# Kernel optimization log

Measured on AMD Instinct MI355X. Metric: run time of the kernel, lower is better.

Reference implementation:

```python
import jax, jax.numpy as jnp
import numpy as np

FDIM = 32
FSIZE = 128          # grid resolution is FSIZE+1 = 129 per axis
N_POINTS = 1048576   # 2**20 query points


def _grid_sample_3d(fm, coords):
    """Trilinear sample of fm [C, D, H, W] at coords [N, 3] in [-1, 1].

    Matches torch F.grid_sample(align_corners=True, padding_mode='border'):
    coords[:, 0] indexes W (x), coords[:, 1] indexes H (y), coords[:, 2] indexes D (z).
    Returns [N, C].
    """
    C, D, H, W = fm.shape

    def prep(c, size):
        # align_corners=True unnormalization, then border clamp
        i = jnp.clip((c + 1.0) * 0.5 * (size - 1), 0.0, size - 1.0)
        i0 = jnp.floor(i)
        idx0 = i0.astype(jnp.int32)
        idx1 = jnp.minimum(idx0 + 1, size - 1)
        return idx0, idx1, i - i0  # frac in [0, 1)

    x0, x1, tx = prep(coords[:, 0], W)
    y0, y1, ty = prep(coords[:, 1], H)
    z0, z1, tz = prep(coords[:, 2], D)

    flat = fm.reshape(C, D * H * W).T  # [D*H*W, C] for point-major gathers

    def gather(zi, yi, xi):
        return jnp.take(flat, (zi * H + yi) * W + xi, axis=0)  # [N, C]

    wx0, wx1 = (1.0 - tx)[:, None], tx[:, None]
    wy0, wy1 = (1.0 - ty)[:, None], ty[:, None]
    wz0, wz1 = (1.0 - tz)[:, None], tz[:, None]

    out = (gather(z0, y0, x0) * (wz0 * wy0 * wx0)
           + gather(z0, y0, x1) * (wz0 * wy0 * wx1)
           + gather(z0, y1, x0) * (wz0 * wy1 * wx0)
           + gather(z0, y1, x1) * (wz0 * wy1 * wx1)
           + gather(z1, y0, x0) * (wz1 * wy0 * wx0)
           + gather(z1, y0, x1) * (wz1 * wy0 * wx1)
           + gather(z1, y1, x0) * (wz1 * wy1 * wx0)
           + gather(z1, y1, x1) * (wz1 * wy1 * wx1))
    return out  # [N, C]


def setup_inputs() -> dict:
    key = jax.random.key(0)
    k1, k2 = jax.random.split(key)
    x = jax.random.uniform(k1, (N_POINTS, 3), jnp.float32, -1.0, 1.0)
    fm = jax.random.normal(k2, (FDIM, FSIZE + 1, FSIZE + 1, FSIZE + 1), jnp.float32) * 0.01
    return {"x": x, "fm": fm}


def reference(x, fm):
    # FeatureVolume.forward with x.shape[1] == 3: returns [N, fdim]
    return _grid_sample_3d(fm, x)
```

## Files before the change

### kernel.cpp

```cpp
#include <hip/hip_runtime.h>
#include <hip/hip_bf16.h>
#include <stdint.h>


#define GRIDW 129
#define S_TOTAL (129 * 129 * 129)
#define NCH 32

typedef float f32x4 __attribute__((ext_vector_type(4)));

static __device__ __forceinline__ ushort f32_to_bf16_rne(float f) {
    uint32_t u = __float_as_uint(f);
    u += 0x7FFFu + ((u >> 16) & 1u);
    return (ushort)(u >> 16);
}

__global__ __launch_bounds__(256) void fv_transpose(const float* __restrict__ fm,
                                                    ushort* __restrict__ vol) {
    __shared__ float tile[256 * 33];
    const int tid = threadIdx.x;
    const int s0 = blockIdx.x * 256;
    const int s = min(s0 + tid, S_TOTAL - 1);
    const float* p = fm + s;
#pragma unroll
    for (int c = 0; c < NCH; ++c) {
        tile[tid * 33 + c] = __builtin_nontemporal_load(p);
        p += S_TOTAL;
    }
    __syncthreads();
    const int sl = tid >> 2;
    const int c0 = (tid & 3) * 8;
#pragma unroll
    for (int k = 0; k < 4; ++k) {
        const int srow = k * 64 + sl;
        const int sg = s0 + srow;
        if (sg < S_TOTAL) {
            uint32_t w[4];
#pragma unroll
            for (int j = 0; j < 4; ++j) {
                const ushort lo = f32_to_bf16_rne(tile[srow * 33 + c0 + 2 * j]);
                const ushort hi = f32_to_bf16_rne(tile[srow * 33 + c0 + 2 * j + 1]);
                w[j] = (uint32_t)lo | ((uint32_t)hi << 16);
            }
            *reinterpret_cast<uint4*>(vol + (size_t)sg * NCH + c0) =
                make_uint4(w[0], w[1], w[2], w[3]);
        }
    }
}

static __device__ __forceinline__ void bf16x4_to_f(uint2 q, float f[4]) {
    f[0] = __uint_as_float(q.x << 16);
    f[1] = __uint_as_float(q.x & 0xFFFF0000u);
    f[2] = __uint_as_float(q.y << 16);
    f[3] = __uint_as_float(q.y & 0xFFFF0000u);
}

__global__ __launch_bounds__(256) void fv_sample(const float* __restrict__ x,
                                                 const ushort* __restrict__ vol,
                                                 float* __restrict__ out,
                                                 int npts) {
    const int gid = blockIdx.x * 256 + threadIdx.x;
    const int p = gid >> 3;
    if (p >= npts) return;
    const int lane8 = gid & 7;

    const float cx = x[3 * p + 0];
    const float cy = x[3 * p + 1];
    const float cz = x[3 * p + 2];

    const float fx = fminf(fmaxf((cx + 1.0f) * 0.5f * 128.0f, 0.0f), 128.0f);
    const float fy = fminf(fmaxf((cy + 1.0f) * 0.5f * 128.0f, 0.0f), 128.0f);
    const float fz = fminf(fmaxf((cz + 1.0f) * 0.5f * 128.0f, 0.0f), 128.0f);

    const float fx0 = floorf(fx), fy0 = floorf(fy), fz0 = floorf(fz);
    const int ix0 = (int)fx0, iy0 = (int)fy0, iz0 = (int)fz0;
    const float tx = fx - fx0, ty = fy - fy0, tz = fz - fz0;
    const uint32_t dX = (ix0 < GRIDW - 1) ? 8u : 0u;
    const uint32_t dY = (iy0 < GRIDW - 1) ? (GRIDW * 8u) : 0u;
    const uint32_t dZ = (iz0 < GRIDW - 1) ? (GRIDW * GRIDW * 8u) : 0u;

    const uint32_t o000 = (uint32_t)((iz0 * GRIDW + iy0) * GRIDW + ix0) * 8u + (uint32_t)lane8;
    const uint32_t o001 = o000 + dX;
    const uint32_t o010 = o000 + dY;
    const uint32_t o011 = o010 + dX;
    const uint32_t o100 = o000 + dZ;
    const uint32_t o101 = o100 + dX;
    const uint32_t o110 = o100 + dY;
    const uint32_t o111 = o110 + dX;

    const uint2* __restrict__ vp = reinterpret_cast<const uint2*>(vol);
    const uint2 q000 = vp[o000];
    const uint2 q001 = vp[o001];
    const uint2 q010 = vp[o010];
    const uint2 q011 = vp[o011];
    const uint2 q100 = vp[o100];
    const uint2 q101 = vp[o101];
    const uint2 q110 = vp[o110];
    const uint2 q111 = vp[o111];

    const float wx1 = tx, wx0 = 1.0f - tx;
    const float wy1 = ty, wy0 = 1.0f - ty;
    const float wz1 = tz, wz0 = 1.0f - tz;
    const float wzy00 = wz0 * wy0, wzy01 = wz0 * wy1;
    const float wzy10 = wz1 * wy0, wzy11 = wz1 * wy1;
    const float w000 = wzy00 * wx0, w001 = wzy00 * wx1;
    const float w010 = wzy01 * wx0, w011 = wzy01 * wx1;
    const float w100 = wzy10 * wx0, w101 = wzy10 * wx1;
    const float w110 = wzy11 * wx0, w111 = wzy11 * wx1;

    float f[4], acc[4];
    bf16x4_to_f(q000, f);
#pragma unroll
    for (int j = 0; j < 4; ++j) acc[j] = w000 * f[j];
    bf16x4_to_f(q001, f);
#pragma unroll
    for (int j = 0; j < 4; ++j) acc[j] += w001 * f[j];
    bf16x4_to_f(q010, f);
#pragma unroll
    for (int j = 0; j < 4; ++j) acc[j] += w010 * f[j];
    bf16x4_to_f(q011, f);
#pragma unroll
    for (int j = 0; j < 4; ++j) acc[j] += w011 * f[j];
    bf16x4_to_f(q100, f);
#pragma unroll
    for (int j = 0; j < 4; ++j) acc[j] += w100 * f[j];
    bf16x4_to_f(q101, f);
#pragma unroll
    for (int j = 0; j < 4; ++j) acc[j] += w101 * f[j];
    bf16x4_to_f(q110, f);
#pragma unroll
    for (int j = 0; j < 4; ++j) acc[j] += w110 * f[j];
    bf16x4_to_f(q111, f);
#pragma unroll
    for (int j = 0; j < 4; ++j) acc[j] += w111 * f[j];

    f32x4 r = {acc[0], acc[1], acc[2], acc[3]};
    f32x4* dst = reinterpret_cast<f32x4*>(out + (size_t)p * NCH) + lane8;
    __builtin_nontemporal_store(r, dst);
}

__global__ __launch_bounds__(256) void fv_sample_direct(const float* __restrict__ x,
                                                        const float* __restrict__ fm,
                                                        float* __restrict__ out,
                                                        int npts) {
    const int gid = blockIdx.x * 256 + threadIdx.x;
    const int p = gid >> 5;
    if (p >= npts) return;
    const int c = gid & 31;

    const float cx = x[3 * p + 0];
    const float cy = x[3 * p + 1];
    const float cz = x[3 * p + 2];

    const float fx = fminf(fmaxf((cx + 1.0f) * 0.5f * 128.0f, 0.0f), 128.0f);
    const float fy = fminf(fmaxf((cy + 1.0f) * 0.5f * 128.0f, 0.0f), 128.0f);
    const float fz = fminf(fmaxf((cz + 1.0f) * 0.5f * 128.0f, 0.0f), 128.0f);

    const float fx0 = floorf(fx), fy0 = floorf(fy), fz0 = floorf(fz);
    const int ix0 = (int)fx0, iy0 = (int)fy0, iz0 = (int)fz0;
    const float tx = fx - fx0, ty = fy - fy0, tz = fz - fz0;
    const int dX = (ix0 < GRIDW - 1) ? 1 : 0;
    const int dY = (iy0 < GRIDW - 1) ? GRIDW : 0;
    const int dZ = (iz0 < GRIDW - 1) ? (GRIDW * GRIDW) : 0;

    const int s000 = (iz0 * GRIDW + iy0) * GRIDW + ix0;
    const float* b = fm + (size_t)c * S_TOTAL;
    const float v000 = b[s000];
    const float v001 = b[s000 + dX];
    const float v010 = b[s000 + dY];
    const float v011 = b[s000 + dY + dX];
    const float v100 = b[s000 + dZ];
    const float v101 = b[s000 + dZ + dX];
    const float v110 = b[s000 + dZ + dY];
    const float v111 = b[s000 + dZ + dY + dX];

    const float wx1 = tx, wx0 = 1.0f - tx;
    const float wy1 = ty, wy0 = 1.0f - ty;
    const float wz1 = tz, wz0 = 1.0f - tz;

    const float r = v000 * (wz0 * wy0 * wx0) + v001 * (wz0 * wy0 * wx1) +
                    v010 * (wz0 * wy1 * wx0) + v011 * (wz0 * wy1 * wx1) +
                    v100 * (wz1 * wy0 * wx0) + v101 * (wz1 * wy0 * wx1) +
                    v110 * (wz1 * wy1 * wx0) + v111 * (wz1 * wy1 * wx1);

    out[(size_t)p * NCH + c] = r;
}

extern "C" void kernel_launch(void* const* d_in, const int* in_sizes, int n_in,
                              void* d_out, int out_size, void* d_ws, size_t ws_size,
                              hipStream_t stream) {
    const float* x = (const float*)d_in[0];
    const float* fm = (const float*)d_in[1];
    float* out = (float*)d_out;
    const int npts = in_sizes[0] / 3;

    const size_t need = (size_t)S_TOTAL * NCH * sizeof(ushort);
    if (ws_size >= need) {
        const int tb = (S_TOTAL + 255) / 256;
        fv_transpose<<<tb, 256, 0, stream>>>(fm, (ushort*)d_ws);
        const int nthreads = npts * 8;
        fv_sample<<<(nthreads + 255) / 256, 256, 0, stream>>>(
            x, (const ushort*)d_ws, out, npts);
    } else {
        const int nthreads = npts * 32;
        fv_sample_direct<<<(nthreads + 255) / 256, 256, 0, stream>>>(x, fm, out, npts);
    }
}
```

Baseline: 523.1 us.

## Sort query points into Morton-ordered spatial buckets before trilinear sampling

```diff
diff --git a/kernel.cpp b/kernel.cpp
--- a/kernel.cpp
+++ b/kernel.cpp
@@ -6,6 +6,8 @@
 #define GRIDW 129
 #define S_TOTAL (129 * 129 * 129)
 #define NCH 32
+#define NB 32768
+#define NXCD 8
 
 typedef float f32x4 __attribute__((ext_vector_type(4)));
 
@@ -15,10 +17,40 @@
     return (ushort)(u >> 16);
 }
 
+static __device__ __forceinline__ uint32_t part1by2(uint32_t x) {
+    x &= 0x3ffu;
+    x = (x | (x << 16)) & 0x30000FFu;
+    x = (x | (x << 8))  & 0x300F00Fu;
+    x = (x | (x << 4))  & 0x30C30C3u;
+    x = (x | (x << 2))  & 0x9249249u;
+    return x;
+}
+
+static __device__ __forceinline__ void prep_coords(float cx, float cy, float cz,
+                                                   int& ix0, int& iy0, int& iz0,
+                                                   float& tx, float& ty, float& tz) {
+    const float fx = fminf(fmaxf((cx + 1.0f) * 0.5f * 128.0f, 0.0f), 128.0f);
+    const float fy = fminf(fmaxf((cy + 1.0f) * 0.5f * 128.0f, 0.0f), 128.0f);
+    const float fz = fminf(fmaxf((cz + 1.0f) * 0.5f * 128.0f, 0.0f), 128.0f);
+    const float fx0 = floorf(fx), fy0 = floorf(fy), fz0 = floorf(fz);
+    ix0 = (int)fx0; iy0 = (int)fy0; iz0 = (int)fz0;
+    tx = fx - fx0; ty = fy - fy0; tz = fz - fz0;
+}
+
+static __device__ __forceinline__ uint32_t bucket_of(int ix0, int iy0, int iz0) {
+    const uint32_t bx = min((uint32_t)ix0 >> 2, 31u);
+    const uint32_t by = min((uint32_t)iy0 >> 2, 31u);
+    const uint32_t bz = min((uint32_t)iz0 >> 2, 31u);
+    return (part1by2(bz) << 2) | (part1by2(by) << 1) | part1by2(bx);
+}
+
 __global__ __launch_bounds__(256) void fv_transpose(const float* __restrict__ fm,
-                                                    ushort* __restrict__ vol) {
+                                                    ushort* __restrict__ vol,
+                                                    uint32_t* __restrict__ hist) {
+    const int tid = threadIdx.x;
+    if (blockIdx.x < NB / 256) hist[blockIdx.x * 256 + tid] = 0;
+
     __shared__ float tile[256 * 33];
-    const int tid = threadIdx.x;
     const int s0 = blockIdx.x * 256;
     const int s = min(s0 + tid, S_TOTAL - 1);
     const float* p = fm + s;
@@ -48,6 +80,52 @@
     }
 }
 
+__global__ __launch_bounds__(256) void fv_hist(const float* __restrict__ x,
+                                               uint32_t* __restrict__ hist,
+                                               ushort* __restrict__ bkt, int npts) {
+    const int p = blockIdx.x * 256 + threadIdx.x;
+    if (p >= npts) return;
+    int ix0, iy0, iz0; float tx, ty, tz;
+    prep_coords(x[3 * p], x[3 * p + 1], x[3 * p + 2], ix0, iy0, iz0, tx, ty, tz);
+    const uint32_t b = bucket_of(ix0, iy0, iz0);
+    bkt[p] = (ushort)b;
+    atomicAdd(&hist[b], 1u);
+}
+
+__global__ __launch_bounds__(1024) void fv_scan(const uint32_t* __restrict__ hist,
+                                                uint32_t* __restrict__ cursor) {
+    __shared__ uint32_t part[1024];
+    const int t = threadIdx.x;
+    const int base = t * (NB / 1024);
+    uint32_t l[NB / 1024];
+    uint32_t s = 0;
+#pragma unroll
+    for (int k = 0; k < NB / 1024; ++k) { l[k] = hist[base + k]; s += l[k]; }
+    part[t] = s;
+    __syncthreads();
+    for (int off = 1; off < 1024; off <<= 1) {
+        const uint32_t v = (t >= off) ? part[t - off] : 0u;
+        __syncthreads();
+        part[t] += v;
+        __syncthreads();
+    }
+    uint32_t run = part[t] - s;
+#pragma unroll
+    for (int k = 0; k < NB / 1024; ++k) { cursor[base + k] = run; run += l[k]; }
+}
+
+__global__ __launch_bounds__(256) void fv_scatter(const float* __restrict__ x,
+                                                  const ushort* __restrict__ bkt,
+                                                  uint32_t* __restrict__ cursor,
+                                                  f32x4* __restrict__ srt, int npts) {
+    const int p = blockIdx.x * 256 + threadIdx.x;
+    if (p >= npts) return;
+    const uint32_t b = bkt[p];
+    const uint32_t pos = atomicAdd(&cursor[b], 1u);
+    f32x4 v = {x[3 * p], x[3 * p + 1], x[3 * p + 2], __uint_as_float((uint32_t)p)};
+    srt[pos] = v;
+}
+
 static __device__ __forceinline__ void bf16x4_to_f(uint2 q, float f[4]) {
     f[0] = __uint_as_float(q.x << 16);
     f[1] = __uint_as_float(q.x & 0xFFFF0000u);
@@ -55,26 +133,26 @@
     f[3] = __uint_as_float(q.y & 0xFFFF0000u);
 }
 
-__global__ __launch_bounds__(256) void fv_sample(const float* __restrict__ x,
-                                                 const ushort* __restrict__ vol,
-                                                 float* __restrict__ out,
-                                                 int npts) {
-    const int gid = blockIdx.x * 256 + threadIdx.x;
-    const int p = gid >> 3;
-    if (p >= npts) return;
+__global__ __launch_bounds__(256) void fv_sample_sorted(const f32x4* __restrict__ srt,
+                                                        const ushort* __restrict__ vol,
+                                                        float* __restrict__ out,
+                                                        int npts, int nwg) {
+    const int b = blockIdx.x;
+    const int q = nwg / NXCD, r = nwg % NXCD;
+    const int xcd = b % NXCD, local = b / NXCD;
+    const int swz = (xcd < r) ? (xcd * (q + 1) + local) : (r * (q + 1) + (xcd - r) * q + local);
+
+    const int gid = swz * 256 + threadIdx.x;
+    const int i = gid >> 3;
+    if (i >= npts) return;
     const int lane8 = gid & 7;
 
-    const float cx = x[3 * p + 0];
-    const float cy = x[3 * p + 1];
-    const float cz = x[3 * p + 2];
-
-    const float fx = fminf(fmaxf((cx + 1.0f) * 0.5f * 128.0f, 0.0f), 128.0f);
-    const float fy = fminf(fmaxf((cy + 1.0f) * 0.5f * 128.0f, 0.0f), 128.0f);
-    const float fz = fminf(fmaxf((cz + 1.0f) * 0.5f * 128.0f, 0.0f), 128.0f);
-
-    const float fx0 = floorf(fx), fy0 = floorf(fy), fz0 = floorf(fz);
-    const int ix0 = (int)fx0, iy0 = (int)fy0, iz0 = (int)fz0;
-    const float tx = fx - fx0, ty = fy - fy0, tz = fz - fz0;
+    const f32x4 rec = srt[i];
+    const uint32_t p = __float_as_uint(rec.w);
+
+    int ix0, iy0, iz0; float tx, ty, tz;
+    prep_coords(rec.x, rec.y, rec.z, ix0, iy0, iz0, tx, ty, tz);
+
     const uint32_t dX = (ix0 < GRIDW - 1) ? 8u : 0u;
     const uint32_t dY = (iy0 < GRIDW - 1) ? (GRIDW * 8u) : 0u;
     const uint32_t dZ = (iz0 < GRIDW - 1) ? (GRIDW * GRIDW * 8u) : 0u;
@@ -134,9 +212,9 @@
 #pragma unroll
     for (int j = 0; j < 4; ++j) acc[j] += w111 * f[j];
 
-    f32x4 r = {acc[0], acc[1], acc[2], acc[3]};
+    f32x4 res = {acc[0], acc[1], acc[2], acc[3]};
     f32x4* dst = reinterpret_cast<f32x4*>(out + (size_t)p * NCH) + lane8;
-    __builtin_nontemporal_store(r, dst);
+    __builtin_nontemporal_store(res, dst);
 }
 
 __global__ __launch_bounds__(256) void fv_sample_direct(const float* __restrict__ x,
@@ -147,22 +225,11 @@
     const int p = gid >> 5;
     if (p >= npts) return;
     const int c = gid & 31;
-
-    const float cx = x[3 * p + 0];
-    const float cy = x[3 * p + 1];
-    const float cz = x[3 * p + 2];
-
-    const float fx = fminf(fmaxf((cx + 1.0f) * 0.5f * 128.0f, 0.0f), 128.0f);
-    const float fy = fminf(fmaxf((cy + 1.0f) * 0.5f * 128.0f, 0.0f), 128.0f);
-    const float fz = fminf(fmaxf((cz + 1.0f) * 0.5f * 128.0f, 0.0f), 128.0f);
-
-    const float fx0 = floorf(fx), fy0 = floorf(fy), fz0 = floorf(fz);
-    const int ix0 = (int)fx0, iy0 = (int)fy0, iz0 = (int)fz0;
-    const float tx = fx - fx0, ty = fy - fy0, tz = fz - fz0;
+    int ix0, iy0, iz0; float tx, ty, tz;
+    prep_coords(x[3 * p], x[3 * p + 1], x[3 * p + 2], ix0, iy0, iz0, tx, ty, tz);
     const int dX = (ix0 < GRIDW - 1) ? 1 : 0;
     const int dY = (iy0 < GRIDW - 1) ? GRIDW : 0;
     const int dZ = (iz0 < GRIDW - 1) ? (GRIDW * GRIDW) : 0;
-
     const int s000 = (iz0 * GRIDW + iy0) * GRIDW + ix0;
     const float* b = fm + (size_t)c * S_TOTAL;
     const float v000 = b[s000];
@@ -173,16 +240,13 @@
     const float v101 = b[s000 + dZ + dX];
     const float v110 = b[s000 + dZ + dY];
     const float v111 = b[s000 + dZ + dY + dX];
-
     const float wx1 = tx, wx0 = 1.0f - tx;
     const float wy1 = ty, wy0 = 1.0f - ty;
     const float wz1 = tz, wz0 = 1.0f - tz;
-
     const float r = v000 * (wz0 * wy0 * wx0) + v001 * (wz0 * wy0 * wx1) +
                     v010 * (wz0 * wy1 * wx0) + v011 * (wz0 * wy1 * wx1) +
                     v100 * (wz1 * wy0 * wx0) + v101 * (wz1 * wy0 * wx1) +
                     v110 * (wz1 * wy1 * wx0) + v111 * (wz1 * wy1 * wx1);
-
     out[(size_t)p * NCH + c] = r;
 }
 
@@ -194,13 +258,23 @@
     float* out = (float*)d_out;
     const int npts = in_sizes[0] / 3;
 
-    const size_t need = (size_t)S_TOTAL * NCH * sizeof(ushort);
+    const size_t HIST_OFF = 144u * 1024u * 1024u;
+    const size_t need = HIST_OFF + 8u * 1024u * 1024u + (size_t)npts * 16u;
     if (ws_size >= need) {
+        ushort* vol = (ushort*)d_ws;
+        uint32_t* hist = (uint32_t*)((char*)d_ws + HIST_OFF);
+        uint32_t* cursor = (uint32_t*)((char*)d_ws + HIST_OFF + (size_t)NB * 4u);
+        ushort* bkt = (ushort*)((char*)d_ws + HIST_OFF + 2u * 1024u * 1024u);
+        f32x4* srt = (f32x4*)((char*)d_ws + HIST_OFF + 8u * 1024u * 1024u);
+
         const int tb = (S_TOTAL + 255) / 256;
-        fv_transpose<<<tb, 256, 0, stream>>>(fm, (ushort*)d_ws);
-        const int nthreads = npts * 8;
-        fv_sample<<<(nthreads + 255) / 256, 256, 0, stream>>>(
-            x, (const ushort*)d_ws, out, npts);
+        fv_transpose<<<tb, 256, 0, stream>>>(fm, vol, hist);
+        const int pb = (npts + 255) / 256;
+        fv_hist<<<pb, 256, 0, stream>>>(x, hist, bkt, npts);
+        fv_scan<<<1, 1024, 0, stream>>>(hist, cursor);
+        fv_scatter<<<pb, 256, 0, stream>>>(x, bkt, cursor, srt, npts);
+        const int nwg = (npts * 8 + 255) / 256;
+        fv_sample_sorted<<<nwg, 256, 0, stream>>>(srt, vol, out, npts, nwg);
     } else {
         const int nthreads = npts * 32;
         fv_sample_direct<<<(nthreads + 255) / 256, 256, 0, stream>>>(x, fm, out, npts);
```

Result: slower. 564.4 us (+7.9%).
